# Kernel optimization log

Measured on AMD Instinct MI355X. Metric: run time of the kernel, lower is better.

Reference implementation:

```python
import jax, jax.numpy as jnp
import numpy as np

B, K, NV, H, T = 4, 2, 32, 16, 4096
G = K * NV                 # conv groups = 64
OPG = 2 * (NV + H)         # out channels per group = 96 (instantaneous doubles channels)
TEMPERATURE = 1.0


def setup_inputs() -> dict:
    key = jax.random.key(0)
    k1, k2, k3 = jax.random.split(key, 3)
    x = jax.random.normal(k1, (B, G * H, T), dtype=jnp.float32)
    W = jax.random.normal(k2, (G, OPG, H), dtype=jnp.float32) * (1.0 / np.sqrt(H))
    b = jax.random.normal(k3, (G, OPG), dtype=jnp.float32) * 0.01
    return {"x": x, "W": W, "b": b}


def reference(x, W, b):
    # pad one zero step at end of sequence (ConstantPad1d((0,1),0))
    xp = jnp.pad(x, ((0, 0), (0, 0), (0, 1)))            # (B, G*H, T+1)
    xg = xp.reshape(B, G, H, T + 1)
    # TCN modeled as grouped pointwise conv: per-group linear over channel dim
    y = jnp.einsum('bgdt,god->bgot', xg, W) + b[None, :, :, None]  # (B, G, OPG, T+1)
    # split temporal / instantaneous branches with the causal shift
    y = y.reshape(B * K, NV, 2, NV + H, T + 1)
    xt = y[:, :, 0, :, :-1]                               # (B*K, NV, NV+H, T)
    xi = y[:, :, 1, :, 1:]                                # (B*K, NV, NV+H, T)
    # split attention logits (first NV channels) and context (last H channels)
    ctx = jnp.concatenate([xt[:, :, NV:, :], xi[:, :, NV:, :]], axis=1)   # (B*K, 2*NV, H, T)
    att = jnp.concatenate([xt[:, :, :NV, :], xi[:, :, :NV, :]], axis=2)   # (B*K, NV, 2*NV, T)
    att = jax.nn.softmax(att / TEMPERATURE, axis=2)
    out = jnp.einsum('bijt,bjdt->bidt', att, ctx)         # (B*K, NV, H, T)
    out = out.reshape(B, K * NV * H, T)
    attn = att.reshape(B, K, NV, 2 * NV, T)
    return out, attn
```

## Files before the change

### kernel.cpp

```cpp
#include <hip/hip_runtime.h>
#include <stdint.h>

#define T_   4096
#define XGS  76
#define AIS  66
#define ATS  2112
#define CTS  1056
#define CSB  (8*ATS)
#define RSW  33

typedef _Float16 h2 __attribute__((ext_vector_type(2)));

static __device__ __forceinline__ float dot2(uint32_t a, uint32_t b, float c) {
#if __has_builtin(__builtin_amdgcn_fdot2)
    return __builtin_amdgcn_fdot2(__builtin_bit_cast(h2, a), __builtin_bit_cast(h2, b), c, false);
#else
    h2 ha = __builtin_bit_cast(h2, a), hb = __builtin_bit_cast(h2, b);
    return fmaf((float)ha.x, (float)hb.x, fmaf((float)ha.y, (float)hb.y, c));
#endif
}
static __device__ __forceinline__ float exp2a(float x) {
#if __has_builtin(__builtin_amdgcn_exp2f)
    return __builtin_amdgcn_exp2f(x);
#else
    return exp2f(x);
#endif
}
static __device__ __forceinline__ uint16_t f2h(float f) {
    _Float16 h = (_Float16)f; return __builtin_bit_cast(uint16_t, h);
}
static __device__ __forceinline__ float h2f(uint16_t u) {
    return (float)__builtin_bit_cast(_Float16, u);
}
static __device__ __forceinline__ uint32_t pk2(float lo, float hi) {
    return __builtin_bit_cast(uint32_t, __builtin_amdgcn_cvt_pkrtz(lo, hi));
}
static __device__ __forceinline__ int stg_idx(int row, int col) {
    return row * 9 + (row >> 4) + col;
}

__global__ __launch_bounds__(512, 2)
void tamcad_kernel(const float* __restrict__ x, const float* __restrict__ W,
                   const float* __restrict__ bias, float* __restrict__ out)
{
    __shared__ uint32_t stg[4640];
    __shared__ uint16_t ACs[CSB + 8*CTS];
    __shared__ float    rs[8 * RSW];

    uint32_t* xs32 = stg;

    const int tid   = threadIdx.x;
    const int bk    = blockIdx.x >> 6;
    const int chunk = blockIdx.x & 63;
    const int b     = bk >> 1;
    const int k     = bk & 1;

    const int oq   = tid & 15;
    const int g    = tid >> 4;
    const int slot = oq >> 3;
    const int dl   = oq;

    uint32_t wp2[6][8];
    float breg[6];
    int sbase[6], sstr[6]; bool isl[6];
    #pragma unroll
    for (int r = 0; r < 6; ++r) {
        const int o = oq * 6 + r;
        const float4* wp = reinterpret_cast<const float4*>(W + (((size_t)(k * 32 + g)) * 96 + o) * 16);
        float4 w0 = wp[0], w1 = wp[1], w2 = wp[2], w3 = wp[3];
        wp2[r][0] = pk2(w0.x, w0.y); wp2[r][1] = pk2(w0.z, w0.w);
        wp2[r][2] = pk2(w1.x, w1.y); wp2[r][3] = pk2(w1.z, w1.w);
        wp2[r][4] = pk2(w2.x, w2.y); wp2[r][5] = pk2(w2.z, w2.w);
        wp2[r][6] = pk2(w3.x, w3.y); wp2[r][7] = pk2(w3.z, w3.w);
        breg[r] = bias[(k * 32 + g) * 96 + o];
        if (o < 32)      { isl[r] = true;  sbase[r] = g * AIS + o;               sstr[r] = ATS; }
        else if (o < 48) { isl[r] = false; sbase[r] = CSB + (o - 32) * AIS + g;  sstr[r] = CTS; }
        else if (o < 80) { isl[r] = true;  sbase[r] = g * AIS + (o - 16);        sstr[r] = ATS; }
        else             { isl[r] = false; sbase[r] = CSB + (o - 80) * AIS + 32 + g; sstr[r] = CTS; }
    }

    const float* xrow = x + ((size_t)b * 1024 + (size_t)(k * 32 + g) * 16 + dl) * (size_t)T_;

    float4 pA, pB; float pS;
    {
        const float* gp = xrow + chunk * 64;
        pA = *(const float4*)(gp + 0);
        pB = *(const float4*)(gp + 4);
        pS = gp[8];
    }

    for (int l = 0; l < 8; ++l) {
        const int t0 = chunk * 64 + l * 8;

        {
            float vals[9] = { pA.x, pA.y, pA.z, pA.w, pB.x, pB.y, pB.z, pB.w, pS };
            #pragma unroll
            for (int i = 0; i < 9; ++i) {
                float mine  = vals[i];
                float other = __shfl_xor(mine, 1);
                if (((i ^ dl) & 1) == 0) {
                    uint32_t pk = (dl & 1) ? pk2(other, mine) : pk2(mine, other);
                    xs32[g * XGS + i * 8 + (dl >> 1)] = pk;
                }
            }
        }
        __syncthreads();

        {
            float asum[8];
            #pragma unroll
            for (int q = 0; q < 8; ++q) {
                const uint32_t* xp = xs32 + g * XGS + (q + slot) * 8;
                uint4 xa = *(const uint4*)xp;
                uint4 xb = *(const uint4*)(xp + 4);
                uint32_t xw[8] = { xa.x, xa.y, xa.z, xa.w, xb.x, xb.y, xb.z, xb.w };
                float s = 0.0f;
                #pragma unroll
                for (int r = 0; r < 6; ++r) {
                    float a = breg[r];
                    #pragma unroll
                    for (int dd = 0; dd < 8; ++dd) a = dot2(wp2[r][dd], xw[dd], a);
                    const float ev = exp2a(fmaf(a, 1.44269504089f, -4.0f));
                    s += isl[r] ? ev : 0.0f;
                    ACs[sbase[r] + q * sstr[r]] = f2h(isl[r] ? ev : a);
                }
                asum[q] = s;
            }
            #pragma unroll
            for (int sft = 1; sft < 16; sft <<= 1) {
                #pragma unroll
                for (int q = 0; q < 8; ++q) asum[q] += __shfl_xor(asum[q], sft);
            }
            if (oq == 0) {
                #pragma unroll
                for (int q = 0; q < 8; ++q)
                    rs[q * RSW + g] = __builtin_amdgcn_rcpf(asum[q]);
            }
        }
        __syncthreads();

        if (l < 7) {
            const int t0n = t0 + 8;
            const float* gp = xrow + t0n;
            pA = *(const float4*)(gp + 0);
            pB = *(const float4*)(gp + 4);
            pS = ((t0n + 8) < T_) ? gp[8] : 0.0f;
        }

        {
            const int t  = tid >> 6;
            const int r6 = tid & 63;
            const int i0 = (r6 & 15) * 2;
            const int d0 = (r6 >> 4) * 4;
            const uint32_t* Aw = (const uint32_t*)ACs;
            const uint32_t* Cw = (const uint32_t*)(ACs + CSB);
            const int abase = t * 1056 + i0 * 33;
            const int cbase = t * 528 + d0 * 33;
            float acc[2][4];
            #pragma unroll
            for (int ii = 0; ii < 2; ++ii)
                #pragma unroll
                for (int dd = 0; dd < 4; ++dd) acc[ii][dd] = 0.f;
            #pragma unroll 8
            for (int jp = 0; jp < 32; ++jp) {
                uint32_t a0 = Aw[abase + jp],      a1 = Aw[abase + 33 + jp];
                uint32_t c0 = Cw[cbase + jp],      c1 = Cw[cbase + 33 + jp];
                uint32_t c2 = Cw[cbase + 66 + jp], c3 = Cw[cbase + 99 + jp];
                acc[0][0] = dot2(a0, c0, acc[0][0]); acc[0][1] = dot2(a0, c1, acc[0][1]);
                acc[0][2] = dot2(a0, c2, acc[0][2]); acc[0][3] = dot2(a0, c3, acc[0][3]);
                acc[1][0] = dot2(a1, c0, acc[1][0]); acc[1][1] = dot2(a1, c1, acc[1][1]);
                acc[1][2] = dot2(a1, c2, acc[1][2]); acc[1][3] = dot2(a1, c3, acc[1][3]);
            }
            const float r0 = rs[t * RSW + i0], r1 = rs[t * RSW + i0 + 1];
            #pragma unroll
            for (int ii = 0; ii < 2; ++ii) {
                const float rv = ii ? r1 : r0;
                #pragma unroll
                for (int dd = 0; dd < 4; ++dd) {
                    const int row = (i0 + ii) * 16 + d0 + dd;
                    stg[stg_idx(row, t)] = __builtin_bit_cast(uint32_t, acc[ii][dd] * rv);
                }
            }
        }
        __syncthreads();

        {
            const int base = stg_idx(tid, 0);
            float ov[8];
            #pragma unroll
            for (int u = 0; u < 8; ++u) ov[u] = __builtin_bit_cast(float, stg[base + u]);
            float* op = out + ((size_t)b * 1024 + k * 512 + tid) * (size_t)T_ + t0;
            *(float4*)(op + 0) = make_float4(ov[0], ov[1], ov[2], ov[3]);
            *(float4*)(op + 4) = make_float4(ov[4], ov[5], ov[6], ov[7]);

            const int j   = tid & 63;
            const int i0a = (tid >> 6) * 4;
            float* attn_base = out + (size_t)4 * 1024 * (size_t)T_;
            #pragma unroll
            for (int ii = 0; ii < 4; ++ii) {
                const int i = i0a + ii;
                float av[8];
                #pragma unroll
                for (int u = 0; u < 8; ++u)
                    av[u] = h2f(ACs[u * ATS + i * AIS + j]) * rs[u * RSW + i];
                float* tp2 = attn_base + (((size_t)bk * 32 + i) * 64 + j) * (size_t)T_ + t0;
                *(float4*)(tp2 + 0) = make_float4(av[0], av[1], av[2], av[3]);
                *(float4*)(tp2 + 4) = make_float4(av[4], av[5], av[6], av[7]);
            }
        }
        __syncthreads();
    }
}

extern "C" void kernel_launch(void* const* d_in, const int* in_sizes, int n_in,
                              void* d_out, int out_size, void* d_ws, size_t ws_size,
                              hipStream_t stream) {
    const float* x  = (const float*)d_in[0];
    const float* W  = (const float*)d_in[1];
    const float* bs = (const float*)d_in[2];
    float* out = (float*)d_out;
    tamcad_kernel<<<dim3(512), dim3(512), 0, stream>>>(x, W, bs, out);
}
```

Before: 288.0 us.

## Warp-specialize attention writeback and context matmul, pipeline across steps

```diff
diff --git a/kernel.cpp b/kernel.cpp
--- a/kernel.cpp
+++ b/kernel.cpp
@@ -1,13 +1,12 @@
 #include <hip/hip_runtime.h>
 #include <stdint.h>
 
-#define T_   4096
-#define XGS  76
-#define AIS  66
-#define ATS  2112
-#define CTS  1056
-#define CSB  (8*ATS)
-#define RSW  33
+#define T_    4096
+#define XGS   74
+#define AIS32 33
+#define ATS32 1056
+#define CTS16 1056
+#define RSW   33
 
 typedef _Float16 h2 __attribute__((ext_vector_type(2)));
 
@@ -35,19 +34,20 @@
 static __device__ __forceinline__ uint32_t pk2(float lo, float hi) {
     return __builtin_bit_cast(uint32_t, __builtin_amdgcn_cvt_pkrtz(lo, hi));
 }
-static __device__ __forceinline__ int stg_idx(int row, int col) {
-    return row * 9 + (row >> 4) + col;
+static __device__ __forceinline__ int stg_ix(int rp, int t) {
+    return rp * 9 + 2 * (rp >> 4) + t;
 }
 
 __global__ __launch_bounds__(512, 2)
 void tamcad_kernel(const float* __restrict__ x, const float* __restrict__ W,
                    const float* __restrict__ bias, float* __restrict__ out)
 {
-    __shared__ uint32_t stg[4640];
-    __shared__ uint16_t ACs[CSB + 8*CTS];
-    __shared__ float    rs[8 * RSW];
-
-    uint32_t* xs32 = stg;
+    __shared__ uint32_t As32[8448];
+    __shared__ uint32_t Cs32[4224];
+    __shared__ uint32_t xs32[2368];
+    __shared__ uint32_t stg [2336];
+    __shared__ float    rs  [264];
+    uint16_t* Cs16 = (uint16_t*)Cs32;
 
     const int tid   = threadIdx.x;
     const int bk    = blockIdx.x >> 6;
@@ -58,71 +58,156 @@
     const int oq   = tid & 15;
     const int g    = tid >> 4;
     const int slot = oq >> 3;
-    const int dl   = oq;
-
-    uint32_t wp2[6][8];
-    float breg[6];
-    int sbase[6], sstr[6]; bool isl[6];
+
+    uint32_t wp2[6][8]; float breg[6]; bool isl[6];
+    int cofs[6]; int aofs[3]; bool acat[3];
     #pragma unroll
     for (int r = 0; r < 6; ++r) {
         const int o = oq * 6 + r;
-        const float4* wp = reinterpret_cast<const float4*>(W + (((size_t)(k * 32 + g)) * 96 + o) * 16);
+        const float4* wp = reinterpret_cast<const float4*>(W + (((size_t)(k*32+g))*96 + o)*16);
         float4 w0 = wp[0], w1 = wp[1], w2 = wp[2], w3 = wp[3];
         wp2[r][0] = pk2(w0.x, w0.y); wp2[r][1] = pk2(w0.z, w0.w);
         wp2[r][2] = pk2(w1.x, w1.y); wp2[r][3] = pk2(w1.z, w1.w);
         wp2[r][4] = pk2(w2.x, w2.y); wp2[r][5] = pk2(w2.z, w2.w);
         wp2[r][6] = pk2(w3.x, w3.y); wp2[r][7] = pk2(w3.z, w3.w);
-        breg[r] = bias[(k * 32 + g) * 96 + o];
-        if (o < 32)      { isl[r] = true;  sbase[r] = g * AIS + o;               sstr[r] = ATS; }
-        else if (o < 48) { isl[r] = false; sbase[r] = CSB + (o - 32) * AIS + g;  sstr[r] = CTS; }
-        else if (o < 80) { isl[r] = true;  sbase[r] = g * AIS + (o - 16);        sstr[r] = ATS; }
-        else             { isl[r] = false; sbase[r] = CSB + (o - 80) * AIS + 32 + g; sstr[r] = CTS; }
-    }
-
-    const float* xrow = x + ((size_t)b * 1024 + (size_t)(k * 32 + g) * 16 + dl) * (size_t)T_;
+        breg[r] = bias[(k*32+g)*96 + o];
+        cofs[r] = 0;
+        if (o < 32)       isl[r] = true;
+        else if (o < 48) { isl[r] = false; cofs[r] = (o-32)*66 + g; }
+        else if (o < 80)  isl[r] = true;
+        else             { isl[r] = false; cofs[r] = (o-80)*66 + 32 + g; }
+    }
+    #pragma unroll
+    for (int p = 0; p < 3; ++p) {
+        const int oe = oq*6 + 2*p;
+        if (oe < 32)                   { acat[p] = true;  aofs[p] = g*AIS32 + (oe >> 1); }
+        else if (oe >= 48 && oe < 80)  { acat[p] = true;  aofs[p] = g*AIS32 + ((oe-16) >> 1); }
+        else                           { acat[p] = false; aofs[p] = 0; }
+    }
+
+    const float* xrow = x + ((size_t)b*1024 + (size_t)(k*32+g)*16 + oq) * (size_t)T_;
 
     float4 pA, pB; float pS;
     {
-        const float* gp = xrow + chunk * 64;
-        pA = *(const float4*)(gp + 0);
-        pB = *(const float4*)(gp + 4);
-        pS = gp[8];
-    }
-
-    for (int l = 0; l < 8; ++l) {
-        const int t0 = chunk * 64 + l * 8;
-
-        {
-            float vals[9] = { pA.x, pA.y, pA.z, pA.w, pB.x, pB.y, pB.z, pB.w, pS };
+        const float* gp = xrow + chunk*64;
+        pA = *(const float4*)gp; pB = *(const float4*)(gp + 4); pS = gp[8];
+    }
+
+    for (int l = 0; l <= 8; ++l) {
+        const int t0p = chunk*64 + (l-1)*8;
+
+        if (l > 0) {
+            if (tid >= 256) {
+                const int q = tid - 256, j = q & 63, jb = j >> 1, jh = j & 1;
+                float* attn_base = out + (size_t)4*1024*(size_t)T_;
+                #pragma unroll
+                for (int rr = 0; rr < 8; ++rr) {
+                    const int i = (q >> 6) + 4*rr;
+                    float av[8];
+                    #pragma unroll
+                    for (int u = 0; u < 8; ++u) {
+                        uint32_t w = As32[u*ATS32 + i*AIS32 + jb];
+                        av[u] = h2f(jh ? (uint16_t)(w >> 16) : (uint16_t)(w & 0xFFFF))
+                              * rs[u*RSW + i];
+                    }
+                    float* tp2 = attn_base + (((size_t)bk*32 + i)*64 + j)*(size_t)T_ + t0p;
+                    *(float4*)(tp2+0) = make_float4(av[0],av[1],av[2],av[3]);
+                    *(float4*)(tp2+4) = make_float4(av[4],av[5],av[6],av[7]);
+                }
+            } else {
+                const int t  = tid >> 5;
+                const int r5 = tid & 31;
+                const int i0 = (r5 >> 2) * 4;
+                const int d0 = (r5 & 3) * 4;
+                const int ab = t*ATS32 + i0*AIS32;
+                const int cb = t*528 + d0*33;
+                float acc[4][4];
+                #pragma unroll
+                for (int ii = 0; ii < 4; ++ii)
+                    #pragma unroll
+                    for (int dd = 0; dd < 4; ++dd) acc[ii][dd] = 0.f;
+                #pragma unroll 4
+                for (int jp = 0; jp < 32; ++jp) {
+                    uint32_t a0 = As32[ab+jp],    a1 = As32[ab+33+jp];
+                    uint32_t a2 = As32[ab+66+jp], a3 = As32[ab+99+jp];
+                    uint32_t c0 = Cs32[cb+jp],    c1 = Cs32[cb+33+jp];
+                    uint32_t c2 = Cs32[cb+66+jp], c3 = Cs32[cb+99+jp];
+                    acc[0][0]=dot2(a0,c0,acc[0][0]); acc[0][1]=dot2(a0,c1,acc[0][1]);
+                    acc[0][2]=dot2(a0,c2,acc[0][2]); acc[0][3]=dot2(a0,c3,acc[0][3]);
+                    acc[1][0]=dot2(a1,c0,acc[1][0]); acc[1][1]=dot2(a1,c1,acc[1][1]);
+                    acc[1][2]=dot2(a1,c2,acc[1][2]); acc[1][3]=dot2(a1,c3,acc[1][3]);
+                    acc[2][0]=dot2(a2,c0,acc[2][0]); acc[2][1]=dot2(a2,c1,acc[2][1]);
+                    acc[2][2]=dot2(a2,c2,acc[2][2]); acc[2][3]=dot2(a2,c3,acc[2][3]);
+                    acc[3][0]=dot2(a3,c0,acc[3][0]); acc[3][1]=dot2(a3,c1,acc[3][1]);
+                    acc[3][2]=dot2(a3,c2,acc[3][2]); acc[3][3]=dot2(a3,c3,acc[3][3]);
+                }
+                #pragma unroll
+                for (int ii = 0; ii < 4; ++ii) {
+                    const float rv = rs[t*RSW + i0 + ii];
+                    const int rp = (i0+ii)*8 + (d0 >> 1);
+                    stg[stg_ix(rp,   t)] = pk2(acc[ii][0]*rv, acc[ii][1]*rv);
+                    stg[stg_ix(rp+1, t)] = pk2(acc[ii][2]*rv, acc[ii][3]*rv);
+                }
+            }
+        }
+        if (l < 8) {
+            float vals[9] = { pA.x,pA.y,pA.z,pA.w, pB.x,pB.y,pB.z,pB.w, pS };
             #pragma unroll
             for (int i = 0; i < 9; ++i) {
                 float mine  = vals[i];
                 float other = __shfl_xor(mine, 1);
-                if (((i ^ dl) & 1) == 0) {
-                    uint32_t pk = (dl & 1) ? pk2(other, mine) : pk2(mine, other);
-                    xs32[g * XGS + i * 8 + (dl >> 1)] = pk;
-                }
+                if (((i ^ oq) & 1) == 0) {
+                    uint32_t pk = (oq & 1) ? pk2(other, mine) : pk2(mine, other);
+                    xs32[g*XGS + i*8 + (oq >> 1)] = pk;
+                }
+            }
+            if (l < 7) {
+                const int t0n = chunk*64 + (l+1)*8;
+                const float* gp = xrow + t0n;
+                pA = *(const float4*)gp; pB = *(const float4*)(gp + 4);
+                pS = ((t0n + 8) < T_) ? gp[8] : 0.0f;
             }
         }
         __syncthreads();
 
-        {
+        if (l > 0) {
+            const int rp = tid >> 1, hi = tid & 1, base = stg_ix(rp, 0);
+            float ov[8];
+            #pragma unroll
+            for (int u = 0; u < 8; ++u) {
+                uint32_t w = stg[base + u];
+                ov[u] = h2f(hi ? (uint16_t)(w >> 16) : (uint16_t)(w & 0xFFFF));
+            }
+            float* op = out + ((size_t)b*1024 + k*512 + tid)*(size_t)T_ + t0p;
+            *(float4*)(op+0) = make_float4(ov[0],ov[1],ov[2],ov[3]);
+            *(float4*)(op+4) = make_float4(ov[4],ov[5],ov[6],ov[7]);
+        }
+        if (l < 8) {
             float asum[8];
             #pragma unroll
             for (int q = 0; q < 8; ++q) {
-                const uint32_t* xp = xs32 + g * XGS + (q + slot) * 8;
+                const uint32_t* xp = xs32 + g*XGS + (q + slot)*8;
                 uint4 xa = *(const uint4*)xp;
                 uint4 xb = *(const uint4*)(xp + 4);
-                uint32_t xw[8] = { xa.x, xa.y, xa.z, xa.w, xb.x, xb.y, xb.z, xb.w };
-                float s = 0.0f;
+                uint32_t xw[8] = { xa.x,xa.y,xa.z,xa.w, xb.x,xb.y,xb.z,xb.w };
+                float v[6]; float s = 0.f;
                 #pragma unroll
                 for (int r = 0; r < 6; ++r) {
-                    float a = breg[r];
+                    float y = breg[r];
                     #pragma unroll
-                    for (int dd = 0; dd < 8; ++dd) a = dot2(wp2[r][dd], xw[dd], a);
-                    const float ev = exp2a(fmaf(a, 1.44269504089f, -4.0f));
-                    s += isl[r] ? ev : 0.0f;
-                    ACs[sbase[r] + q * sstr[r]] = f2h(isl[r] ? ev : a);
+                    for (int dd = 0; dd < 8; ++dd) y = dot2(wp2[r][dd], xw[dd], y);
+                    const float e = exp2a(fmaf(y, 1.44269504089f, -4.0f));
+                    v[r] = isl[r] ? e : y;
+                    s   += isl[r] ? e : 0.f;
+                }
+                #pragma unroll
+                for (int p = 0; p < 3; ++p) {
+                    if (acat[p]) {
+                        As32[q*ATS32 + aofs[p]] = pk2(v[2*p], v[2*p+1]);
+                    } else {
+                        Cs16[q*CTS16 + cofs[2*p]]   = f2h(v[2*p]);
+                        Cs16[q*CTS16 + cofs[2*p+1]] = f2h(v[2*p+1]);
+                    }
                 }
                 asum[q] = s;
             }
@@ -134,81 +219,10 @@
             if (oq == 0) {
                 #pragma unroll
                 for (int q = 0; q < 8; ++q)
-                    rs[q * RSW + g] = __builtin_amdgcn_rcpf(asum[q]);
-            }
-        }
-        __syncthreads();
-
-        if (l < 7) {
-            const int t0n = t0 + 8;
-            const float* gp = xrow + t0n;
-            pA = *(const float4*)(gp + 0);
-            pB = *(const float4*)(gp + 4);
-            pS = ((t0n + 8) < T_) ? gp[8] : 0.0f;
-        }
-
-        {
-            const int t  = tid >> 6;
-            const int r6 = tid & 63;
-            const int i0 = (r6 & 15) * 2;
-            const int d0 = (r6 >> 4) * 4;
-            const uint32_t* Aw = (const uint32_t*)ACs;
-            const uint32_t* Cw = (const uint32_t*)(ACs + CSB);
-            const int abase = t * 1056 + i0 * 33;
-            const int cbase = t * 528 + d0 * 33;
-            float acc[2][4];
-            #pragma unroll
-            for (int ii = 0; ii < 2; ++ii)
-                #pragma unroll
-                for (int dd = 0; dd < 4; ++dd) acc[ii][dd] = 0.f;
-            #pragma unroll 8
-            for (int jp = 0; jp < 32; ++jp) {
-                uint32_t a0 = Aw[abase + jp],      a1 = Aw[abase + 33 + jp];
-                uint32_t c0 = Cw[cbase + jp],      c1 = Cw[cbase + 33 + jp];
-                uint32_t c2 = Cw[cbase + 66 + jp], c3 = Cw[cbase + 99 + jp];
-                acc[0][0] = dot2(a0, c0, acc[0][0]); acc[0][1] = dot2(a0, c1, acc[0][1]);
-                acc[0][2] = dot2(a0, c2, acc[0][2]); acc[0][3] = dot2(a0, c3, acc[0][3]);
-                acc[1][0] = dot2(a1, c0, acc[1][0]); acc[1][1] = dot2(a1, c1, acc[1][1]);
-                acc[1][2] = dot2(a1, c2, acc[1][2]); acc[1][3] = dot2(a1, c3, acc[1][3]);
-            }
-            const float r0 = rs[t * RSW + i0], r1 = rs[t * RSW + i0 + 1];
-            #pragma unroll
-            for (int ii = 0; ii < 2; ++ii) {
-                const float rv = ii ? r1 : r0;
-                #pragma unroll
-                for (int dd = 0; dd < 4; ++dd) {
-                    const int row = (i0 + ii) * 16 + d0 + dd;
-                    stg[stg_idx(row, t)] = __builtin_bit_cast(uint32_t, acc[ii][dd] * rv);
-                }
-            }
-        }
-        __syncthreads();
-
-        {
-            const int base = stg_idx(tid, 0);
-            float ov[8];
-            #pragma unroll
-            for (int u = 0; u < 8; ++u) ov[u] = __builtin_bit_cast(float, stg[base + u]);
-            float* op = out + ((size_t)b * 1024 + k * 512 + tid) * (size_t)T_ + t0;
-            *(float4*)(op + 0) = make_float4(ov[0], ov[1], ov[2], ov[3]);
-            *(float4*)(op + 4) = make_float4(ov[4], ov[5], ov[6], ov[7]);
-
-            const int j   = tid & 63;
-            const int i0a = (tid >> 6) * 4;
-            float* attn_base = out + (size_t)4 * 1024 * (size_t)T_;
-            #pragma unroll
-            for (int ii = 0; ii < 4; ++ii) {
-                const int i = i0a + ii;
-                float av[8];
-                #pragma unroll
-                for (int u = 0; u < 8; ++u)
-                    av[u] = h2f(ACs[u * ATS + i * AIS + j]) * rs[u * RSW + i];
-                float* tp2 = attn_base + (((size_t)bk * 32 + i) * 64 + j) * (size_t)T_ + t0;
-                *(float4*)(tp2 + 0) = make_float4(av[0], av[1], av[2], av[3]);
-                *(float4*)(tp2 + 4) = make_float4(av[4], av[5], av[6], av[7]);
-            }
-        }
-        __syncthreads();
+                    rs[q*RSW + g] = __builtin_amdgcn_rcpf(asum[q]);
+            }
+        }
+        if (l < 8) __syncthreads();
     }
 }
 
```

Result: no change. 285.6 us (-0.8%).
